# Kernel tuning notes

Hardware: AMD Instinct MI355X
Metric: run time of the kernel (lower is better)

Reference implementation:

```python
import jax, jax.numpy as jnp
import numpy as np

B, T, V, H, W = 2, 4, 4, 128, 128
NQ = 64
QDIM, IDIM, MDIM = 256, 32, 16

def setup_inputs() -> dict:
    key = jax.random.key(0)
    ks = jax.random.split(key, 9)
    return {
        "instance_affinity": jax.random.normal(ks[0], (B, T, V, H, W, IDIM), dtype=jnp.float32),
        "motion_code": jax.random.normal(ks[1], (B, T, V, H, W, MDIM), dtype=jnp.float32),
        "query_feat": jax.random.normal(ks[2], (B, T, NQ, QDIM), dtype=jnp.float32),
        "assignment_prob": jax.random.uniform(ks[3], (B, T, V, H, W, NQ + 1), dtype=jnp.float32),
        "assigned_query": jax.random.randint(ks[4], (B, T, V, H, W), 0, NQ + 1, dtype=jnp.int64),
        "W_inst": jax.random.normal(ks[5], (QDIM, IDIM), dtype=jnp.float32) * 0.02,
        "b_inst": jax.random.normal(ks[6], (IDIM,), dtype=jnp.float32) * 0.02,
        "W_motion": jax.random.normal(ks[7], (QDIM, MDIM), dtype=jnp.float32) * 0.02,
        "b_motion": jax.random.normal(ks[8], (MDIM,), dtype=jnp.float32) * 0.02,
    }

def reference(instance_affinity, motion_code, query_feat, assignment_prob, assigned_query, W_inst, b_inst, W_motion, b_motion):
    # project queries: (b,t,q,query_dim) -> (b,t,q,d)
    query_inst = query_feat @ W_inst + b_inst      # (b,t,q,32)
    query_motion = query_feat @ W_motion + b_motion  # (b,t,q,16)
    bg_prob = assignment_prob[..., :1]   # (b,t,v,h,w,1)
    fg_prob = assignment_prob[..., 1:]   # (b,t,v,h,w,nq)
    fg_norm = jnp.maximum(fg_prob.sum(axis=-1, keepdims=True), 1e-6)
    # weighted-sum pooling over queries as a fused contraction (no huge broadcast intermediate)
    pooled_inst = jnp.einsum('btvhwq,btqd->btvhwd', fg_prob, query_inst) / fg_norm
    pooled_motion = jnp.einsum('btvhwq,btqd->btvhwd', fg_prob, query_motion) / fg_norm
    refine_gate = 1.0 - bg_prob
    inst = instance_affinity + refine_gate * pooled_inst
    motion = motion_code + refine_gate * pooled_motion
    entity_id = assigned_query  # already (b,t,v,h,w)
    return (entity_id, inst, motion)
```

## Files before the change

kernel.cpp:

```cpp
#include <hip/hip_runtime.h>

#define BT    8
#define VHW   (4*128*128)
#define NQn   64
#define QD    256
#define ID    32
#define MD    16
#define CD    48
#define TILE  256

__global__ __launch_bounds__(256) void qproj_kernel(
    const float* __restrict__ qf,
    const float* __restrict__ Wi,
    const float* __restrict__ bi,
    const float* __restrict__ Wm,
    const float* __restrict__ bm,
    float* __restrict__ qtab)
{
    int idx = blockIdx.x * 256 + threadIdx.x;
    int btq = idx / CD;
    int d   = idx - btq * CD;
    const float* __restrict__ qrow = qf + btq * QD;
    float a;
    if (d < ID) {
        a = bi[d];
        #pragma unroll 8
        for (int k = 0; k < QD; ++k) a = fmaf(qrow[k], Wi[k*ID + d], a);
    } else {
        int dm = d - ID;
        a = bm[dm];
        #pragma unroll 8
        for (int k = 0; k < QD; ++k) a = fmaf(qrow[k], Wm[k*MD + dm], a);
    }
    qtab[idx] = a;
}

__global__ __launch_bounds__(256) void entity_kernel(
    const float* __restrict__ ia,
    const float* __restrict__ mc,
    const float* __restrict__ ap,
    const int*   __restrict__ aq,
    const float* __restrict__ qtab,
    float* __restrict__ out_id,
    float* __restrict__ out_inst,
    float* __restrict__ out_mot)
{
    __shared__ float ap_s[TILE * (NQn + 1)];

    const int  bt   = blockIdx.x >> 8;
    const long base = (long)blockIdx.x * TILE;
    const int  t    = threadIdx.x;

    {
        const float4* __restrict__ src = (const float4*)(ap + base * (NQn + 1));
        float4* dst = (float4*)ap_s;
        #pragma unroll
        for (int f = t, k = 0; k < 17; ++k, f += 256)
            if (f < (TILE * (NQn + 1)) / 4) dst[f] = src[f];
    }
    __syncthreads();

    const long loc = base + t;
    const float* __restrict__ qt    = qtab + bt * (NQn * CD);
    const float* __restrict__ aprow = ap_s + t * (NQn + 1);

    float acc[CD];
    #pragma unroll
    for (int d = 0; d < CD; ++d) acc[d] = 0.0f;

    const float bg = aprow[0];
    float psum = 0.0f;

    #pragma unroll 4
    for (int q = 0; q < NQn; ++q) {
        float p = aprow[1 + q];
        psum += p;
        const float* __restrict__ row = qt + q * CD;
        #pragma unroll
        for (int d = 0; d < CD; ++d) acc[d] = fmaf(p, row[d], acc[d]);
    }

    const float scale = (1.0f - bg) / fmaxf(psum, 1e-6f);

    const float4* __restrict__ ia4 = (const float4*)(ia + loc * ID);
    float4* __restrict__ oi4 = (float4*)(out_inst + loc * ID);
    #pragma unroll
    for (int i = 0; i < ID/4; ++i) {
        float4 v = ia4[i];
        v.x = fmaf(scale, acc[4*i+0], v.x);
        v.y = fmaf(scale, acc[4*i+1], v.y);
        v.z = fmaf(scale, acc[4*i+2], v.z);
        v.w = fmaf(scale, acc[4*i+3], v.w);
        oi4[i] = v;
    }
    const float4* __restrict__ mc4 = (const float4*)(mc + loc * MD);
    float4* __restrict__ om4 = (float4*)(out_mot + loc * MD);
    #pragma unroll
    for (int i = 0; i < MD/4; ++i) {
        float4 v = mc4[i];
        v.x = fmaf(scale, acc[ID+4*i+0], v.x);
        v.y = fmaf(scale, acc[ID+4*i+1], v.y);
        v.z = fmaf(scale, acc[ID+4*i+2], v.z);
        v.w = fmaf(scale, acc[ID+4*i+3], v.w);
        om4[i] = v;
    }

    out_id[loc] = (float)aq[loc];
}

extern "C" void kernel_launch(void* const* d_in, const int* in_sizes, int n_in,
                              void* d_out, int out_size, void* d_ws, size_t ws_size,
                              hipStream_t stream) {
    const float* ia = (const float*)d_in[0];
    const float* mc = (const float*)d_in[1];
    const float* qf = (const float*)d_in[2];
    const float* ap = (const float*)d_in[3];
    const int*   aq = (const int*)  d_in[4];
    const float* Wi = (const float*)d_in[5];
    const float* bi = (const float*)d_in[6];
    const float* Wm = (const float*)d_in[7];
    const float* bm = (const float*)d_in[8];

    float* qtab = (float*)d_ws;

    float* out_id   = (float*)d_out;
    float* out_inst = out_id + (long)BT * VHW;
    float* out_mot  = out_inst + (long)BT * VHW * ID;

    qproj_kernel<<<(BT * NQn * CD) / 256, 256, 0, stream>>>(qf, Wi, bi, Wm, bm, qtab);
    entity_kernel<<<(BT * VHW) / TILE, TILE, 0, stream>>>(ia, mc, ap, aq, qtab,
                                                          out_id, out_inst, out_mot);
}
```

Baseline: 378.6 us.

## Compute query pooling with bf16 MFMA instead of scalar FMA loops

Replaces the per-thread 64x48 scalar FMA loop with 16x16x32 bf16 MFMA instructions. The projected query table is written pre-swizzled in bf16 fragment layout, and assignment probabilities are converted to bf16 in a padded shared-memory tile. The probability sum is computed by an extra MFMA against a ones column. This removes the VALU-bound contraction and the redundant global reads of the query table per pixel, at the cost of bf16 precision on probabilities and query projections. Output stores become scalar 16-lane strided writes instead of float4.

Result: faster. 343.1 us (-9.4%).

```diff
diff --git a/kernel.cpp b/kernel.cpp
--- a/kernel.cpp
+++ b/kernel.cpp
@@ -7,7 +7,17 @@
 #define ID    32
 #define MD    16
 #define CD    48
-#define TILE  256
+#define APW   65
+#define PITCH 72
+
+typedef short bf16x8 __attribute__((ext_vector_type(8)));
+typedef float f32x4  __attribute__((ext_vector_type(4)));
+
+static __device__ __forceinline__ short f2bf(float f) {
+    unsigned u = __builtin_bit_cast(unsigned, f);
+    unsigned r = (u + 0x7FFFu + ((u >> 16) & 1u)) >> 16;
+    return (short)r;
+}
 
 __global__ __launch_bounds__(256) void qproj_kernel(
     const float* __restrict__ qf,
@@ -15,11 +25,13 @@
     const float* __restrict__ bi,
     const float* __restrict__ Wm,
     const float* __restrict__ bm,
-    float* __restrict__ qtab)
+    short* __restrict__ qtabB)
 {
     int idx = blockIdx.x * 256 + threadIdx.x;
     int btq = idx / CD;
     int d   = idx - btq * CD;
+    int bt  = btq >> 6;
+    int q   = btq & 63;
     const float* __restrict__ qrow = qf + btq * QD;
     float a;
     if (d < ID) {
@@ -32,7 +44,11 @@
         #pragma unroll 8
         for (int k = 0; k < QD; ++k) a = fmaf(qrow[k], Wm[k*MD + dm], a);
     }
-    qtab[idx] = a;
+    int nt = d >> 4, c = d & 15;
+    int kt = q >> 5, kk = q & 31;
+    int lane = ((kk >> 3) << 4) | c;
+    int j    = kk & 7;
+    qtabB[((((bt*3 + nt)*2 + kt) << 6) + lane) * 8 + j] = f2bf(a);
 }
 
 __global__ __launch_bounds__(256) void entity_kernel(
@@ -40,72 +56,108 @@
     const float* __restrict__ mc,
     const float* __restrict__ ap,
     const int*   __restrict__ aq,
-    const float* __restrict__ qtab,
+    const short* __restrict__ qtabB,
     float* __restrict__ out_id,
     float* __restrict__ out_inst,
     float* __restrict__ out_mot)
 {
-    __shared__ float ap_s[TILE * (NQn + 1)];
+    __shared__ short ap_s[256 * PITCH];
+    __shared__ float bg_s[256];
+    __shared__ float psum_s[256];
+    __shared__ float scale_s[256];
 
+    const int  t    = threadIdx.x;
+    const int  lane = t & 63;
+    const int  w    = t >> 6;
     const int  bt   = blockIdx.x >> 8;
-    const long base = (long)blockIdx.x * TILE;
-    const int  t    = threadIdx.x;
+    const long base = (long)blockIdx.x << 8;
 
     {
-        const float4* __restrict__ src = (const float4*)(ap + base * (NQn + 1));
-        float4* dst = (float4*)ap_s;
+        const float4* __restrict__ src = (const float4*)(ap + base * APW);
         #pragma unroll
-        for (int f = t, k = 0; k < 17; ++k, f += 256)
-            if (f < (TILE * (NQn + 1)) / 4) dst[f] = src[f];
+        for (int k = 0; k < 17; ++k) {
+            int f = t + 256 * k;
+            if (f < (256 * APW) / 4) {
+                float4 v = src[f];
+                int e0 = 4 * f;
+                #pragma unroll
+                for (int e = 0; e < 4; ++e) {
+                    int   ix  = e0 + e;
+                    int   loc = ix / APW;
+                    int   col = ix - loc * APW;
+                    float val = (&v.x)[e];
+                    if (col == 0) bg_s[loc] = val;
+                    else          ap_s[loc * PITCH + (col - 1)] = f2bf(val);
+                }
+            }
+        }
+    }
+
+    bf16x8 Bf[3][2];
+    {
+        const bf16x8* __restrict__ qb = (const bf16x8*)(qtabB + bt * (3*2*64*8));
+        #pragma unroll
+        for (int nt = 0; nt < 3; ++nt)
+            #pragma unroll
+            for (int kt = 0; kt < 2; ++kt)
+                Bf[nt][kt] = qb[(nt*2 + kt) * 64 + lane];
+    }
+    bf16x8 Bones;
+    {
+        short one = ((lane & 15) == 0) ? (short)0x3F80 : (short)0;
+        #pragma unroll
+        for (int j = 0; j < 8; ++j) Bones[j] = one;
+    }
+
+    __syncthreads();
+
+    f32x4 acc[4][3];
+    f32x4 accP[4];
+    #pragma unroll
+    for (int m = 0; m < 4; ++m) {
+        accP[m] = (f32x4){0.f, 0.f, 0.f, 0.f};
+        #pragma unroll
+        for (int n = 0; n < 3; ++n) acc[m][n] = (f32x4){0.f, 0.f, 0.f, 0.f};
+    }
+    #pragma unroll
+    for (int kt = 0; kt < 2; ++kt) {
+        #pragma unroll
+        for (int m = 0; m < 4; ++m) {
+            const bf16x8 A = *(const bf16x8*)(ap_s +
+                (w*64 + m*16 + (lane & 15)) * PITCH + kt*32 + ((lane >> 4) << 3));
+            acc[m][0] = __builtin_amdgcn_mfma_f32_16x16x32_bf16(A, Bf[0][kt], acc[m][0], 0, 0, 0);
+            acc[m][1] = __builtin_amdgcn_mfma_f32_16x16x32_bf16(A, Bf[1][kt], acc[m][1], 0, 0, 0);
+            acc[m][2] = __builtin_amdgcn_mfma_f32_16x16x32_bf16(A, Bf[2][kt], acc[m][2], 0, 0, 0);
+            accP[m]   = __builtin_amdgcn_mfma_f32_16x16x32_bf16(A, Bones,     accP[m],   0, 0, 0);
+        }
+    }
+
+    if ((lane & 15) == 0) {
+        int g = lane >> 4;
+        #pragma unroll
+        for (int m = 0; m < 4; ++m)
+            #pragma unroll
+            for (int r = 0; r < 4; ++r)
+                psum_s[w*64 + m*16 + g*4 + r] = accP[m][r];
     }
     __syncthreads();
+    scale_s[t] = (1.0f - bg_s[t]) / fmaxf(psum_s[t], 1e-6f);
+    __syncthreads();
 
-    const long loc = base + t;
-    const float* __restrict__ qt    = qtab + bt * (NQn * CD);
-    const float* __restrict__ aprow = ap_s + t * (NQn + 1);
-
-    float acc[CD];
+    const int c = lane & 15, g = lane >> 4;
     #pragma unroll
-    for (int d = 0; d < CD; ++d) acc[d] = 0.0f;
-
-    const float bg = aprow[0];
-    float psum = 0.0f;
-
-    #pragma unroll 4
-    for (int q = 0; q < NQn; ++q) {
-        float p = aprow[1 + q];
-        psum += p;
-        const float* __restrict__ row = qt + q * CD;
+    for (int m = 0; m < 4; ++m) {
+        const int lrow = w*64 + m*16 + g*4;
         #pragma unroll
-        for (int d = 0; d < CD; ++d) acc[d] = fmaf(p, row[d], acc[d]);
+        for (int r = 0; r < 4; ++r) {
+            const long  loc = base + lrow + r;
+            const float s   = scale_s[lrow + r];
+            out_inst[loc*ID + c]      = ia[loc*ID + c]      + s * acc[m][0][r];
+            out_inst[loc*ID + 16 + c] = ia[loc*ID + 16 + c] + s * acc[m][1][r];
+            out_mot [loc*MD + c]      = mc[loc*MD + c]      + s * acc[m][2][r];
+        }
     }
-
-    const float scale = (1.0f - bg) / fmaxf(psum, 1e-6f);
-
-    const float4* __restrict__ ia4 = (const float4*)(ia + loc * ID);
-    float4* __restrict__ oi4 = (float4*)(out_inst + loc * ID);
-    #pragma unroll
-    for (int i = 0; i < ID/4; ++i) {
-        float4 v = ia4[i];
-        v.x = fmaf(scale, acc[4*i+0], v.x);
-        v.y = fmaf(scale, acc[4*i+1], v.y);
-        v.z = fmaf(scale, acc[4*i+2], v.z);
-        v.w = fmaf(scale, acc[4*i+3], v.w);
-        oi4[i] = v;
-    }
-    const float4* __restrict__ mc4 = (const float4*)(mc + loc * MD);
-    float4* __restrict__ om4 = (float4*)(out_mot + loc * MD);
-    #pragma unroll
-    for (int i = 0; i < MD/4; ++i) {
-        float4 v = mc4[i];
-        v.x = fmaf(scale, acc[ID+4*i+0], v.x);
-        v.y = fmaf(scale, acc[ID+4*i+1], v.y);
-        v.z = fmaf(scale, acc[ID+4*i+2], v.z);
-        v.w = fmaf(scale, acc[ID+4*i+3], v.w);
-        om4[i] = v;
-    }
-
-    out_id[loc] = (float)aq[loc];
+    out_id[base + t] = (float)aq[base + t];
 }
 
 extern "C" void kernel_launch(void* const* d_in, const int* in_sizes, int n_in,
@@ -121,13 +173,13 @@
     const float* Wm = (const float*)d_in[7];
     const float* bm = (const float*)d_in[8];
 
-    float* qtab = (float*)d_ws;
+    short* qtabB = (short*)d_ws;
 
     float* out_id   = (float*)d_out;
     float* out_inst = out_id + (long)BT * VHW;
     float* out_mot  = out_inst + (long)BT * VHW * ID;
 
-    qproj_kernel<<<(BT * NQn * CD) / 256, 256, 0, stream>>>(qf, Wi, bi, Wm, bm, qtab);
-    entity_kernel<<<(BT * VHW) / TILE, TILE, 0, stream>>>(ia, mc, ap, aq, qtab,
-                                                          out_id, out_inst, out_mot);
+    qproj_kernel<<<(BT * NQn * CD) / 256, 256, 0, stream>>>(qf, Wi, bi, Wm, bm, qtabB);
+    entity_kernel<<<(BT * VHW) / 256, 256, 0, stream>>>(ia, mc, ap, aq, qtabB,
+                                                        out_id, out_inst, out_mot);
 }
```
